# Performance work log

Measured on AMD Instinct MI355X. Metric: run time of the kernel, lower is better.

## Reference

```python
import jax, jax.numpy as jnp
import numpy as np

B, H, W, C = 8, 64, 64, 128
L = H * W
NH = 4
HD = C // NH
SCALE = HD ** -0.5
WIN = 8
SHIFT = 4
DEPTH = 2
K = 3
N = WIN * WIN
NW = (H // WIN) * (W // WIN)


def _rel_pos_index(win):
    coords = np.stack(np.meshgrid(np.arange(win), np.arange(win), indexing='ij'))
    cf = coords.reshape(2, -1)
    rel = (cf[:, :, None] - cf[:, None, :]).transpose(1, 2, 0).copy()
    rel[:, :, 0] += win - 1
    rel[:, :, 1] += win - 1
    rel[:, :, 0] *= 2 * win - 1
    return rel.sum(-1)  # (N, N)

REL_IDX = jnp.asarray(_rel_pos_index(WIN).reshape(-1))


def _attn_mask(Hh, Ww, win, shift):
    img = np.zeros((Hh, Ww))
    cnt = 0
    for hs in (slice(0, -win), slice(-win, -shift), slice(-shift, None)):
        for ws in (slice(0, -win), slice(-win, -shift), slice(-shift, None)):
            img[hs, ws] = cnt
            cnt += 1
    mw = img.reshape(Hh // win, win, Ww // win, win).transpose(0, 2, 1, 3).reshape(-1, win * win)
    m = mw[:, None, :] - mw[:, :, None]
    return jnp.asarray(np.where(m != 0, -100.0, 0.0).astype(np.float32))  # (nW, N, N)

ATTN_MASK = _attn_mask(H, W, WIN, SHIFT)


def layer_norm(x, g, b, eps=1e-5):
    mu = x.mean(-1, keepdims=True)
    var = x.var(-1, keepdims=True)
    return (x - mu) / jnp.sqrt(var + eps) * g + b


def window_partition(x, win):
    Bb, Hh, Ww, Cc = x.shape
    x = x.reshape(Bb, Hh // win, win, Ww // win, win, Cc)
    return x.transpose(0, 1, 3, 2, 4, 5).reshape(-1, win, win, Cc)


def window_reverse(wins, win, Hh, Ww):
    Bb = wins.shape[0] // (Hh * Ww // win // win)
    x = wins.reshape(Bb, Hh // win, Ww // win, win, win, -1)
    return x.transpose(0, 1, 3, 2, 4, 5).reshape(Bb, Hh, Ww, -1)


def swin_block(x, shift, n1g, n1b, qkvw, qkvb, rp, pw, pb, n2g, n2b, f1w, f1b, f2w, f2b):
    shortcut = x
    x = layer_norm(x, n1g, n1b).reshape(B, H, W, C)
    if shift > 0:
        x = jnp.roll(x, (-shift, -shift), axis=(1, 2))
    xw = window_partition(x, WIN).reshape(-1, N, C)  # (B*nW, N, C)
    qkv = (xw @ qkvw + qkvb).reshape(-1, N, 3, NH, HD).transpose(2, 0, 3, 1, 4)
    q, k, v = qkv[0] * SCALE, qkv[1], qkv[2]
    attn = jnp.einsum('whnd,whmd->whnm', q, k)  # (B*nW, NH, N, N)
    bias = rp[REL_IDX].reshape(N, N, NH).transpose(2, 0, 1)
    attn = attn + bias[None]
    if shift > 0:
        attn = (attn.reshape(B, NW, NH, N, N) + ATTN_MASK[None, :, None]).reshape(-1, NH, N, N)
    attn = jax.nn.softmax(attn, axis=-1)
    out = jnp.einsum('whnm,whmd->whnd', attn, v).transpose(0, 2, 1, 3).reshape(-1, N, C)
    out = out @ pw + pb
    x = window_reverse(out.reshape(-1, WIN, WIN, C), WIN, H, W)
    if shift > 0:
        x = jnp.roll(x, (shift, shift), axis=(1, 2))
    x = shortcut + x.reshape(B, L, C)
    h = layer_norm(x, n2g, n2b)
    h = jax.nn.gelu(h @ f1w + f1b, approximate=False) @ f2w + f2b
    return x + h


def conv1d(x, w, b):  # x (B,C,L), w (O,I,K)
    y = jax.lax.conv_general_dilated(x, w, (1,), [(K // 2, K // 2)], dimension_numbers=('NCH', 'OIH', 'NCH'))
    return y + b[None, :, None]


def deform_conv1d(xt, off_w, off_b, msk_w, msk_b):
    x = xt.transpose(0, 2, 1)  # (B, C, L)
    offset = conv1d(x, off_w, off_b)                    # (B, K, L)
    mask = jax.nn.sigmoid(conv1d(x, msk_w, msk_b))      # (B, K, L)
    i = jnp.arange(L, dtype=x.dtype)
    pos = jnp.clip(i[None, None, :] + offset, 0.0, L - 1)  # (B, K, L)
    fp = jnp.floor(pos).astype(jnp.int32)
    cp = jnp.minimum(fp + 1, L - 1)
    alpha = pos - fp.astype(x.dtype)
    idx_f = jnp.broadcast_to(fp[:, None], (B, C, K, L))
    idx_c = jnp.broadcast_to(cp[:, None], (B, C, K, L))
    xe = jnp.broadcast_to(x[:, :, None, :], (B, C, K, L))
    xf = jnp.take_along_axis(xe, idx_f, axis=3)
    xc = jnp.take_along_axis(xe, idx_c, axis=3)
    samp = xf * (1.0 - alpha[:, None]) + xc * alpha[:, None]
    out = (samp * mask[:, None]).sum(2)  # (B, C, L)
    # faithful to torch: output.view(B, L, out_channels) reinterprets memory, no transpose
    return out.reshape(B, L, C)


def _forward(xt, hx, cx, red_w, red_b, n1g, n1b, qkvw, qkvb, rp, pw, pb, n2g, n2b,
             f1w, f1b, f2w, f2b, off_w, off_b, msk_w, msk_b, lf_w, lf_b, gf_w, gf_b, ff_w, ff_b):
    # global branch: inject hidden state then W-MSA / SW-MSA blocks
    g = jnp.concatenate([xt, hx], axis=-1) @ red_w + red_b
    for i, shift in enumerate((0, SHIFT)):
        g = swin_block(g, shift, n1g[i], n1b[i], qkvw[i], qkvb[i], rp[i], pw[i], pb[i],
                       n2g[i], n2b[i], f1w[i], f1b[i], f2w[i], f2b[i])
    # local branch: deformable 1D conv over token axis
    local = deform_conv1d(xt, off_w, off_b, msk_w, msk_b)
    # local-global fusion
    fu = jax.nn.relu((local @ lf_w + lf_b) * (g @ gf_w + gf_b)) @ ff_w + ff_b
    # LSTM-style gating (SwinLSTM cell update)
    gate = jax.nn.sigmoid(fu)
    cell = jnp.tanh(fu)
    cy = gate * (cx + cell)
    hy = gate * jnp.tanh(cy)
    return hy


def setup_inputs():
    key = jax.random.key(0)
    ks = iter(jax.random.split(key, 24))
    def rn(shape, s=0.02):
        return jax.random.normal(next(ks), shape, jnp.float32) * s
    return dict(
        xt=jax.random.normal(next(ks), (B, L, C), jnp.float32),
        hx=jax.random.normal(next(ks), (B, L, C), jnp.float32),
        cx=jax.random.normal(next(ks), (B, L, C), jnp.float32),
        red_w=rn((2 * C, C)), red_b=jnp.zeros((C,), jnp.float32),
        n1g=jnp.ones((DEPTH, C), jnp.float32), n1b=jnp.zeros((DEPTH, C), jnp.float32),
        qkvw=rn((DEPTH, C, 3 * C)), qkvb=jnp.zeros((DEPTH, 3 * C), jnp.float32),
        rp=rn((DEPTH, (2 * WIN - 1) ** 2, NH)),
        pw=rn((DEPTH, C, C)), pb=jnp.zeros((DEPTH, C), jnp.float32),
        n2g=jnp.ones((DEPTH, C), jnp.float32), n2b=jnp.zeros((DEPTH, C), jnp.float32),
        f1w=rn((DEPTH, C, 4 * C)), f1b=jnp.zeros((DEPTH, 4 * C), jnp.float32),
        f2w=rn((DEPTH, 4 * C, C)), f2b=jnp.zeros((DEPTH, C), jnp.float32),
        off_w=rn((K, C, K)), off_b=jnp.zeros((K,), jnp.float32),
        msk_w=rn((K, C, K)), msk_b=jnp.zeros((K,), jnp.float32),
        lf_w=rn((C, C)), lf_b=jnp.zeros((C,), jnp.float32),
        gf_w=rn((C, C)), gf_b=jnp.zeros((C,), jnp.float32),
        ff_w=rn((C, C)), ff_b=jnp.zeros((C,), jnp.float32),
    )


def reference(xt, hx, cx, red_w, red_b, n1g, n1b, qkvw, qkvb, rp, pw, pb, n2g, n2b,
              f1w, f1b, f2w, f2b, off_w, off_b, msk_w, msk_b, lf_w, lf_b, gf_w, gf_b, ff_w, ff_b):
    return _forward(xt, hx, cx, red_w, red_b, n1g, n1b, qkvw, qkvb, rp, pw, pb, n2g, n2b,
                    f1w, f1b, f2w, f2b, off_w, off_b, msk_w, msk_b, lf_w, lf_b, gf_w, gf_b, ff_w, ff_b)
```

## Files before the change

kernel.cpp:

```cpp
#include <hip/hip_runtime.h>
#include <hip/hip_bf16.h>
#include <math.h>

typedef __hip_bfloat16 bf16;
typedef unsigned short u16;
#define BF(x) __bfloat162float(x)
static __device__ __forceinline__ bf16 FB(float x) { return __float2bfloat16(x); }
static __device__ __forceinline__ u16 FBu(float x) {
    bf16 b = __float2bfloat16(x);
    return *(u16*)&b;
}

typedef __attribute__((ext_vector_type(4))) float f32x4;
typedef __attribute__((ext_vector_type(8))) __bf16 bf16x8;


#define O_REDW 0
#define O_QKVW 32768
#define O_PW   131072
#define O_F1W  163840
#define O_F2W  294912
#define O_LFW  425984
#define O_GFW  442368
#define O_FFW  458752
#define O_REDB 475136
#define O_QKVB 475264
#define O_PB   476032
#define O_F1B  476288
#define O_F2B  477312
#define O_LFB  477568
#define O_GFB  477696
#define O_FFB  477824
#define O_RP   477952
#define O_N1G  479752
#define O_N1B  480008
#define O_N2G  480264
#define O_N2B  480520
#define O_OW   480776
#define O_OB   481928
#define O_MW   481931
#define O_MB   483083

#define ROW_S 36
#define CH_S  2320
#define CH32_S 1168

__device__ __forceinline__ int get_mode(const void* xt) {
    const unsigned* w = (const unsigned*)xt;
    int zlo = 0, inband = 0;
    #pragma unroll
    for (int i = 0; i < 32; ++i) {
        unsigned lo = w[i] & 0xFFFFu;
        int e = (int)((lo >> 7) & 0xFF);
        zlo += (lo == 0u || lo == 0x8000u);
        inband += (e >= 100 && e <= 140);
    }
    if (zlo >= 29) return 1;
    return (inband >= 20) ? 0 : 1;
}

__device__ __forceinline__ float LD(const void* p, size_t i, int mode) {
    return mode ? ((const float*)p)[i] : BF(((const bf16*)p)[i]);
}

__device__ __forceinline__ void async16(const u16* g, u16* l) {
    __builtin_amdgcn_global_load_lds(
        (const __attribute__((address_space(1))) unsigned int*)g,
        (__attribute__((address_space(3))) unsigned int*)l, 16, 0, 0);
}

struct PrepT { const void* src; int srcOff, K, N, dstOff; };
struct Prep { PrepT d[29]; int start[30]; };

__global__ void prep_k(Prep p, bf16* __restrict__ dst, const void* __restrict__ dtp) {
    const int mode = get_mode(dtp);
    int i = blockIdx.x * 256 + threadIdx.x;
    if (i >= p.start[29]) return;
    int s = 0;
    while (p.start[s + 1] <= i) ++s;
    int e = i - p.start[s];
    float v;
    if (p.d[s].N > 0) {
        int n = e / p.d[s].K, k = e % p.d[s].K;
        v = LD(p.d[s].src, (size_t)p.d[s].srcOff + (size_t)k * p.d[s].N + n, mode);
    } else {
        v = LD(p.d[s].src, (size_t)p.d[s].srcOff + e, mode);
    }
    dst[p.d[s].dstOff + e] = FB(v);
}

__launch_bounds__(256)
__global__ void xcat_k(const void* __restrict__ xt, const void* __restrict__ hx,
                       u16* __restrict__ X) {
    const int mode = get_mode(xt);
    const int total = 32768 * 32;
    for (int gidx = blockIdx.x * 256 + threadIdx.x; gidx < total;
         gidx += gridDim.x * 256) {
        int r = gidx >> 5, gi = gidx & 31;
        const void* src = (gi < 16) ? xt : hx;
        int c = (gi & 15) << 3;
        u16 outv[8];
        if (mode) {
            const float* s = (const float*)src + (size_t)r * 128 + c;
            float4 a = *(const float4*)s;
            float4 b = *(const float4*)(s + 4);
            outv[0] = FBu(a.x); outv[1] = FBu(a.y); outv[2] = FBu(a.z); outv[3] = FBu(a.w);
            outv[4] = FBu(b.x); outv[5] = FBu(b.y); outv[6] = FBu(b.z); outv[7] = FBu(b.w);
        } else {
            *(uint4*)outv = *(const uint4*)((const u16*)src + (size_t)r * 128 + c);
        }
        *(uint4*)(X + (size_t)r * 256 + (gi << 3)) = *(const uint4*)outv;
    }
}

template <int EPI>
__launch_bounds__(256)
__global__ void gemm_mfma(const u16* __restrict__ A, const u16* __restrict__ Bt,
                          const bf16* __restrict__ bias, bf16* __restrict__ outb,
                          float* __restrict__ outf, int M, int N, int K, int shift) {
    __shared__ __align__(16) u16 Als[2][2048];
    __shared__ __align__(16) u16 Bls[2][4096];
    const int tid = threadIdx.x;
    const int wave = tid >> 6, lane = tid & 63;
    const int q = lane >> 4, lr = lane & 15;
    const int wm = (wave >> 1) << 5, wn = (wave & 1) << 6;
    const int bm = blockIdx.y << 6, bn = blockIdx.x << 7;
    const f32x4 zero = {0.f, 0.f, 0.f, 0.f};
    f32x4 acc[2][4];
    #pragma unroll
    for (int i = 0; i < 2; ++i)
        #pragma unroll
        for (int j = 0; j < 4; ++j) acc[i][j] = zero;

    const int nk = K >> 5;
    {
        int c = tid;
        async16(A + (size_t)(bm + (c >> 2)) * K + ((c & 3) << 3), Als[0] + (c << 3));
        #pragma unroll
        for (int c2 = tid; c2 < 512; c2 += 256)
            async16(Bt + (size_t)(bn + (c2 >> 2)) * K + ((c2 & 3) << 3), Bls[0] + (c2 << 3));
    }
    __syncthreads();

    for (int i = 0; i < nk; ++i) {
        const int cur = i & 1, nxt = cur ^ 1;
        if (i + 1 < nk) {
            int k1 = (i + 1) << 5;
            int c = tid;
            async16(A + (size_t)(bm + (c >> 2)) * K + k1 + ((c & 3) << 3), Als[nxt] + (c << 3));
            #pragma unroll
            for (int c2 = tid; c2 < 512; c2 += 256)
                async16(Bt + (size_t)(bn + (c2 >> 2)) * K + k1 + ((c2 & 3) << 3), Bls[nxt] + (c2 << 3));
        }
        bf16x8 af[2], bfr[4];
        #pragma unroll
        for (int t = 0; t < 2; ++t)
            af[t] = *(const bf16x8*)(Als[cur] + ((wm + (t << 4) + lr) << 5) + (q << 3));
        #pragma unroll
        for (int t = 0; t < 4; ++t)
            bfr[t] = *(const bf16x8*)(Bls[cur] + ((wn + (t << 4) + lr) << 5) + (q << 3));
        #pragma unroll
        for (int mt = 0; mt < 2; ++mt)
            #pragma unroll
            for (int nt = 0; nt < 4; ++nt)
                acc[mt][nt] = __builtin_amdgcn_mfma_f32_16x16x32_bf16(
                    af[mt], bfr[nt], acc[mt][nt], 0, 0, 0);
        __syncthreads();
    }

    #pragma unroll
    for (int nt = 0; nt < 4; ++nt) {
        int col = bn + wn + (nt << 4) + lr;
        float bv = BF(bias[col]);
        #pragma unroll
        for (int mt = 0; mt < 2; ++mt) {
            int row0 = bm + wm + (mt << 4) + (q << 2);
            #pragma unroll
            for (int i = 0; i < 4; ++i) {
                int r = row0 + i;
                float v = acc[mt][nt][i] + bv;
                size_t idx = (size_t)r * N + col;
                if (EPI == 0) {
                    outb[idx] = FB(v);
                } else if (EPI == 3) {
                    int b = r >> 12, rem = r & 4095;
                    int wi = rem >> 6, n = rem & 63;
                    int hp = ((wi >> 3) << 3) + (n >> 3);
                    int wp = ((wi & 7) << 3) + (n & 7);
                    int h = (hp + shift) & 63, w = (wp + shift) & 63;
                    outf[((size_t)((b << 12) + (h << 6) + w)) * 128 + col] += v;
                } else if (EPI == 5) {
                    outf[idx] = v;
                }
            }
        }
    }
}

__launch_bounds__(256)
__global__ void qkvln_k(const float* __restrict__ g, const u16* __restrict__ wtu,
                        const bf16* __restrict__ wtb, u16* __restrict__ qkv,
                        int d, int shift) {
    __shared__ __align__(16) u16 Ach[4 * CH_S];
    __shared__ __align__(16) u16 Bb[2][8192];
    const int tid = threadIdx.x;
    const int wave = tid >> 6, lane = tid & 63;
    const int q = lane >> 4, lr = lane & 15;
    const int wm = (wave >> 1) << 5, wn = (wave & 1) << 6;
    const int bm = blockIdx.x << 6;
    const u16* Wq = wtu + O_QKVW + d * 49152;

    #pragma unroll
    for (int i = tid; i < 1024; i += 256) {
        int kc = i >> 9, c = i & 511;
        async16(Wq + (size_t)(c >> 2) * 128 + (kc << 5) + ((c & 3) << 3),
                Bb[0] + (kc << 12) + (c << 3));
    }

    {
        int row = tid >> 2, qtr = tid & 3;
        int r = bm + row;
        int b = r >> 12, rem = r & 4095;
        int wi = rem >> 6, n = rem & 63;
        int hp = ((wi >> 3) << 3) + (n >> 3);
        int wp = ((wi & 7) << 3) + (n & 7);
        int h = (hp + shift) & 63, w = (wp + shift) & 63;
        int src = (b << 12) + (h << 6) + w;
        const float* gr = g + (size_t)src * 128 + qtr * 32;
        float vals[32];
        float s1 = 0.f, s2 = 0.f;
        #pragma unroll
        for (int i = 0; i < 8; ++i) {
            float4 v4 = *(const float4*)(gr + i * 4);
            vals[i * 4] = v4.x; vals[i * 4 + 1] = v4.y;
            vals[i * 4 + 2] = v4.z; vals[i * 4 + 3] = v4.w;
            s1 += v4.x + v4.y + v4.z + v4.w;
            s2 += v4.x * v4.x + v4.y * v4.y + v4.z * v4.z + v4.w * v4.w;
        }
        s1 += __shfl_xor(s1, 1); s1 += __shfl_xor(s1, 2);
        s2 += __shfl_xor(s2, 1); s2 += __shfl_xor(s2, 2);
        float mu = s1 * (1.f / 128.f);
        float var = s2 * (1.f / 128.f) - mu * mu;
        float inv = rsqrtf(var + 1e-5f);
        #pragma unroll
        for (int i = 0; i < 32; ++i) {
            int c = qtr * 32 + i;
            float o = (vals[i] - mu) * inv * BF(wtb[O_N1G + d * 128 + c])
                      + BF(wtb[O_N1B + d * 128 + c]);
            Ach[qtr * CH_S + row * ROW_S + i] = FBu(o);
        }
    }
    __syncthreads();

    const f32x4 zero = {0.f, 0.f, 0.f, 0.f};
    f32x4 acc[2][4];
    for (int s = 0; s < 6; ++s) {
        const int nc = s >> 1, kh = s & 1;
        const int bsel = s & 1;
        if (s < 5) {
            int t = s + 1, nct = t >> 1, kht = t & 1;
            const u16* Bg = Wq + nct * 16384;
            #pragma unroll
            for (int i = tid; i < 1024; i += 256) {
                int kc = i >> 9, c = i & 511;
                async16(Bg + (size_t)(c >> 2) * 128 + (kht << 6) + (kc << 5) + ((c & 3) << 3),
                        Bb[t & 1] + (kc << 12) + (c << 3));
            }
        }
        if (kh == 0) {
            #pragma unroll
            for (int i = 0; i < 2; ++i)
                #pragma unroll
                for (int j = 0; j < 4; ++j) acc[i][j] = zero;
        }
        #pragma unroll
        for (int kc = 0; kc < 2; ++kc) {
            bf16x8 af[2], bfr[4];
            #pragma unroll
            for (int t = 0; t < 2; ++t)
                af[t] = *(const bf16x8*)(Ach + (2 * kh + kc) * CH_S + (wm + (t << 4) + lr) * ROW_S + (q << 3));
            #pragma unroll
            for (int t = 0; t < 4; ++t)
                bfr[t] = *(const bf16x8*)(Bb[bsel] + (kc << 12) + ((wn + (t << 4) + lr) << 5) + (q << 3));
            #pragma unroll
            for (int mt = 0; mt < 2; ++mt)
                #pragma unroll
                for (int nt = 0; nt < 4; ++nt)
                    acc[mt][nt] = __builtin_amdgcn_mfma_f32_16x16x32_bf16(
                        af[mt], bfr[nt], acc[mt][nt], 0, 0, 0);
        }
        if (kh == 1) {
            #pragma unroll
            for (int nt = 0; nt < 4; ++nt) {
                int col = wn + (nt << 4) + lr;
                float bv = BF(wtb[O_QKVB + d * 384 + nc * 128 + col]);
                #pragma unroll
                for (int mt = 0; mt < 2; ++mt) {
                    #pragma unroll
                    for (int i = 0; i < 4; ++i) {
                        int r = bm + wm + (mt << 4) + (q << 2) + i;
                        qkv[(size_t)r * 384 + nc * 128 + col] = FBu(acc[mt][nt][i] + bv);
                    }
                }
            }
        }
        if (s < 5) __syncthreads();
    }
}

__launch_bounds__(256, 2)
__global__ void attn_k(const u16* __restrict__ qkv, const bf16* __restrict__ rp,
                       u16* __restrict__ outp, int shift) {
    __shared__ __align__(16) u16 vT[4][32][72];
    __shared__ __align__(16) u16 pbuf[4][64][72];
    const int wq = blockIdx.x;
    const int head = threadIdx.x >> 6;
    const int lane = threadIdx.x & 63;
    const int q8 = lane >> 4, lr = lane & 15;
    const size_t base = (size_t)wq * 64;
    const f32x4 zero = {0.f, 0.f, 0.f, 0.f};

    #pragma unroll
    for (int j = 0; j < 4; ++j) {
        bf16x8 vv = *(const bf16x8*)(qkv + (base + lane) * 384 + 256 + head * 32 + j * 8);
        #pragma unroll
        for (int e = 0; e < 8; ++e) vT[head][j * 8 + e][lane] = ((const u16*)&vv)[e];
    }

    bf16x8 af[4], bfk[4];
    #pragma unroll
    for (int t = 0; t < 4; ++t) {
        af[t]  = *(const bf16x8*)(qkv + (base + t * 16 + lr) * 384 + head * 32 + q8 * 8);
        bfk[t] = *(const bf16x8*)(qkv + (base + t * 16 + lr) * 384 + 128 + head * 32 + q8 * 8);
    }
    f32x4 accs[4][4];
    #pragma unroll
    for (int rt = 0; rt < 4; ++rt)
        #pragma unroll
        for (int ct = 0; ct < 4; ++ct) accs[rt][ct] = zero;
    #pragma unroll
    for (int rt = 0; rt < 4; ++rt)
        #pragma unroll
        for (int ct = 0; ct < 4; ++ct)
            accs[rt][ct] = __builtin_amdgcn_mfma_f32_16x16x32_bf16(
                af[rt], bfk[ct], accs[rt][ct], 0, 0, 0);

    const int wloc = wq & 63;
    const int wh = (wloc >> 3) << 3, wwb = (wloc & 7) << 3;
    #pragma unroll
    for (int rt = 0; rt < 4; ++rt) {
        #pragma unroll
        for (int i = 0; i < 4; ++i) {
            int r = rt * 16 + q8 * 4 + i;
            int ti = r >> 3, tj = r & 7;
            int regt = 0;
            if (shift) {
                int hp = wh + ti, wp = wwb + tj;
                int rh = hp < 56 ? 0 : (hp < 60 ? 1 : 2);
                int rw = wp < 56 ? 0 : (wp < 60 ? 1 : 2);
                regt = rh * 3 + rw;
            }
            float sv[4];
            float mx = -1e30f;
            #pragma unroll
            for (int ct = 0; ct < 4; ++ct) {
                int m = ct * 16 + lr;
                float a = accs[rt][ct][i] * 0.17677669529663687f;
                int idx = (ti - (m >> 3) + 7) * 15 + (tj - (m & 7) + 7);
                a += BF(rp[idx * 4 + head]);
                if (shift) {
                    int hp = wh + (m >> 3), wp = wwb + (m & 7);
                    int rh = hp < 56 ? 0 : (hp < 60 ? 1 : 2);
                    int rw = wp < 56 ? 0 : (wp < 60 ? 1 : 2);
                    if (regt != rh * 3 + rw) a -= 100.f;
                }
                sv[ct] = a;
                mx = fmaxf(mx, a);
            }
            mx = fmaxf(mx, __shfl_xor(mx, 1));
            mx = fmaxf(mx, __shfl_xor(mx, 2));
            mx = fmaxf(mx, __shfl_xor(mx, 4));
            mx = fmaxf(mx, __shfl_xor(mx, 8));
            float l = 0.f;
            #pragma unroll
            for (int ct = 0; ct < 4; ++ct) { sv[ct] = expf(sv[ct] - mx); l += sv[ct]; }
            l += __shfl_xor(l, 1); l += __shfl_xor(l, 2);
            l += __shfl_xor(l, 4); l += __shfl_xor(l, 8);
            float inv = 1.f / l;
            #pragma unroll
            for (int ct = 0; ct < 4; ++ct)
                pbuf[head][r][ct * 16 + lr] = FBu(sv[ct] * inv);
        }
    }

    f32x4 acco[4][2];
    #pragma unroll
    for (int rt = 0; rt < 4; ++rt) { acco[rt][0] = zero; acco[rt][1] = zero; }
    #pragma unroll
    for (int mh = 0; mh < 2; ++mh) {
        bf16x8 vb[2];
        #pragma unroll
        for (int dt = 0; dt < 2; ++dt)
            vb[dt] = *(const bf16x8*)(&vT[head][dt * 16 + lr][mh * 32 + q8 * 8]);
        #pragma unroll
        for (int rt = 0; rt < 4; ++rt) {
            bf16x8 pa = *(const bf16x8*)(&pbuf[head][rt * 16 + lr][mh * 32 + q8 * 8]);
            #pragma unroll
            for (int dt = 0; dt < 2; ++dt)
                acco[rt][dt] = __builtin_amdgcn_mfma_f32_16x16x32_bf16(
                    pa, vb[dt], acco[rt][dt], 0, 0, 0);
        }
    }

    #pragma unroll
    for (int rt = 0; rt < 4; ++rt)
        #pragma unroll
        for (int dt = 0; dt < 2; ++dt)
            #pragma unroll
            for (int i = 0; i < 4; ++i) {
                int r = rt * 16 + q8 * 4 + i;
                outp[(base + r) * 128 + head * 32 + dt * 16 + lr] = FBu(acco[rt][dt][i]);
            }
}

__launch_bounds__(256)
__global__ void mlp_k(float* __restrict__ g, bf16* __restrict__ gbf,
                      const u16* __restrict__ wtu, const bf16* __restrict__ wtb,
                      int d) {
    __shared__ __align__(16) u16 Ach[4 * CH_S];
    __shared__ __align__(16) u16 bufB1[8192];
    __shared__ __align__(16) u16 bufB2[8192];
    __shared__ __align__(16) u16 buf2[2 * CH_S];
    const int tid = threadIdx.x;
    const int wave = tid >> 6, lane = tid & 63;
    const int q = lane >> 4, lr = lane & 15;
    const int wm = (wave >> 1) << 5;
    const int wn0 = (wave & 1) << 5;
    const int wn = (wave & 1) << 6;
    const int bm = blockIdx.x << 6;

    {
        const u16* B1g = wtu + O_F1W + d * 65536;
        #pragma unroll
        for (int i = tid; i < 1024; i += 256) {
            int kc = i >> 8, c = i & 255;
            async16(B1g + (c >> 2) * 128 + (kc << 5) + ((c & 3) << 3),
                    bufB1 + (kc << 11) + (c << 3));
        }
    }

    {
        int row = tid >> 2, qtr = tid & 3;
        const float* gr = g + (size_t)(bm + row) * 128 + qtr * 32;
        float vals[32];
        float s1 = 0.f, s2 = 0.f;
        #pragma unroll
        for (int i = 0; i < 8; ++i) {
            float4 v4 = *(const float4*)(gr + i * 4);
            vals[i * 4] = v4.x; vals[i * 4 + 1] = v4.y;
            vals[i * 4 + 2] = v4.z; vals[i * 4 + 3] = v4.w;
            s1 += v4.x + v4.y + v4.z + v4.w;
            s2 += v4.x * v4.x + v4.y * v4.y + v4.z * v4.z + v4.w * v4.w;
        }
        s1 += __shfl_xor(s1, 1); s1 += __shfl_xor(s1, 2);
        s2 += __shfl_xor(s2, 1); s2 += __shfl_xor(s2, 2);
        float mu = s1 * (1.f / 128.f);
        float var = s2 * (1.f / 128.f) - mu * mu;
        float inv = rsqrtf(var + 1e-5f);
        #pragma unroll
        for (int i = 0; i < 32; ++i) {
            int c = qtr * 32 + i;
            float o = (vals[i] - mu) * inv * BF(wtb[O_N2G + d * 128 + c])
                      + BF(wtb[O_N2B + d * 128 + c]);
            Ach[qtr * CH_S + row * ROW_S + i] = FBu(o);
        }
    }
    __syncthreads();

    const f32x4 zero = {0.f, 0.f, 0.f, 0.f};
    f32x4 acc2[2][4];
    #pragma unroll
    for (int i = 0; i < 2; ++i)
        #pragma unroll
        for (int j = 0; j < 4; ++j) acc2[i][j] = zero;

    for (int h = 0; h < 8; ++h) {
        {
            const u16* B2g = wtu + O_F2W + d * 65536 + h * 64;
            #pragma unroll
            for (int i = tid; i < 1024; i += 256) {
                int kc = i >> 9, c = i & 511;
                async16(B2g + (size_t)(c >> 2) * 512 + (kc << 5) + ((c & 3) << 3),
                        bufB2 + (kc << 12) + (c << 3));
            }
        }
        f32x4 acc1[2][2];
        #pragma unroll
        for (int i = 0; i < 2; ++i) { acc1[i][0] = zero; acc1[i][1] = zero; }
        #pragma unroll
        for (int k0 = 0; k0 < 4; ++k0) {
            bf16x8 af[2], bfr[2];
            #pragma unroll
            for (int t = 0; t < 2; ++t) {
                af[t]  = *(const bf16x8*)(Ach + k0 * CH_S + (wm + (t << 4) + lr) * ROW_S + (q << 3));
                bfr[t] = *(const bf16x8*)(bufB1 + (k0 << 11) + ((wn0 + (t << 4) + lr) << 5) + (q << 3));
            }
            #pragma unroll
            for (int mt = 0; mt < 2; ++mt)
                #pragma unroll
                for (int nt = 0; nt < 2; ++nt)
                    acc1[mt][nt] = __builtin_amdgcn_mfma_f32_16x16x32_bf16(
                        af[mt], bfr[nt], acc1[mt][nt], 0, 0, 0);
        }
        #pragma unroll
        for (int nt = 0; nt < 2; ++nt) {
            int c = wn0 + (nt << 4) + lr;
            float hb = BF(wtb[O_F1B + d * 512 + h * 64 + c]);
            #pragma unroll
            for (int mt = 0; mt < 2; ++mt) {
                #pragma unroll
                for (int i = 0; i < 4; ++i) {
                    int r = wm + (mt << 4) + (q << 2) + i;
                    float v = acc1[mt][nt][i] + hb;
                    float ge = 0.5f * v * (1.0f + erff(v * 0.70710678118654752f));
                    buf2[(c >> 5) * CH_S + r * ROW_S + (c & 31)] = FBu(ge);
                }
            }
        }
        __syncthreads();
        if (h < 7) {
            const u16* B1g = wtu + O_F1W + d * 65536 + (h + 1) * 8192;
            #pragma unroll
            for (int i = tid; i < 1024; i += 256) {
                int kc = i >> 8, c = i & 255;
                async16(B1g + (c >> 2) * 128 + (kc << 5) + ((c & 3) << 3),
                        bufB1 + (kc << 11) + (c << 3));
            }
        }
        #pragma unroll
        for (int kc = 0; kc < 2; ++kc) {
            bf16x8 ah[2], b2[4];
            #pragma unroll
            for (int t = 0; t < 2; ++t)
                ah[t] = *(const bf16x8*)(buf2 + kc * CH_S + (wm + (t << 4) + lr) * ROW_S + (q << 3));
            #pragma unroll
            for (int t = 0; t < 4; ++t)
                b2[t] = *(const bf16x8*)(bufB2 + (kc << 12) + ((wn + (t << 4) + lr) << 5) + (q << 3));
            #pragma unroll
            for (int mt = 0; mt < 2; ++mt)
                #pragma unroll
                for (int nt = 0; nt < 4; ++nt)
                    acc2[mt][nt] = __builtin_amdgcn_mfma_f32_16x16x32_bf16(
                        ah[mt], b2[nt], acc2[mt][nt], 0, 0, 0);
        }
        __syncthreads();
    }
    #pragma unroll
    for (int nt = 0; nt < 4; ++nt) {
        int col = wn + (nt << 4) + lr;
        float bv = BF(wtb[O_F2B + d * 128 + col]);
        #pragma unroll
        for (int mt = 0; mt < 2; ++mt) {
            #pragma unroll
            for (int i = 0; i < 4; ++i) {
                int r = bm + wm + (mt << 4) + (q << 2) + i;
                size_t idx = (size_t)r * 128 + col;
                float nv = g[idx] + acc2[mt][nt][i] + bv;
                g[idx] = nv;
                gbf[idx] = FB(nv);
            }
        }
    }
}

__launch_bounds__(256, 4)
__global__ void fuse3_k(const u16* __restrict__ Aloc, const u16* __restrict__ Ag,
                        const u16* __restrict__ wtu, const bf16* __restrict__ wtb,
                        const void* __restrict__ cx, void* __restrict__ out,
                        const void* __restrict__ dtp) {
    __shared__ __align__(16) u16 relb[4 * CH32_S];
    const int mode = get_mode(dtp);
    const int tid = threadIdx.x;
    const int wave = tid >> 6, lane = tid & 63;
    const int q = lane >> 4, lr = lane & 15;
    const int wn = wave << 5;
    const int bm = blockIdx.x << 5;
    const f32x4 zero = {0.f, 0.f, 0.f, 0.f};
    f32x4 acc1[2][2], acc2[2][2];
    #pragma unroll
    for (int i = 0; i < 2; ++i)
        #pragma unroll
        for (int j = 0; j < 2; ++j) { acc1[i][j] = zero; acc2[i][j] = zero; }

    #pragma unroll
    for (int k0 = 0; k0 < 4; ++k0) {
        bf16x8 al[2], ag[2], blf[2], bgf[2];
        #pragma unroll
        for (int t = 0; t < 2; ++t) {
            size_t off = (size_t)(bm + (t << 4) + lr) * 128 + (k0 << 5) + (q << 3);
            al[t] = *(const bf16x8*)(Aloc + off);
            ag[t] = *(const bf16x8*)(Ag + off);
        }
        #pragma unroll
        for (int t = 0; t < 2; ++t) {
            int woff = ((wn + (t << 4) + lr) << 7) + (k0 << 5) + (q << 3);
            blf[t] = *(const bf16x8*)(wtu + O_LFW + woff);
            bgf[t] = *(const bf16x8*)(wtu + O_GFW + woff);
        }
        #pragma unroll
        for (int mt = 0; mt < 2; ++mt)
            #pragma unroll
            for (int nt = 0; nt < 2; ++nt) {
                acc1[mt][nt] = __builtin_amdgcn_mfma_f32_16x16x32_bf16(
                    al[mt], blf[nt], acc1[mt][nt], 0, 0, 0);
                acc2[mt][nt] = __builtin_amdgcn_mfma_f32_16x16x32_bf16(
                    ag[mt], bgf[nt], acc2[mt][nt], 0, 0, 0);
            }
    }
    #pragma unroll
    for (int nt = 0; nt < 2; ++nt) {
        int c = wn + (nt << 4) + lr;
        float lfb = BF(wtb[O_LFB + c]);
        float gfb = BF(wtb[O_GFB + c]);
        #pragma unroll
        for (int mt = 0; mt < 2; ++mt) {
            #pragma unroll
            for (int i = 0; i < 4; ++i) {
                int r = (mt << 4) + (q << 2) + i;
                float t1 = acc1[mt][nt][i] + lfb;
                float t2 = acc2[mt][nt][i] + gfb;
                float rel = t1 * t2;
                relb[(c >> 5) * CH32_S + r * ROW_S + (c & 31)] = FBu(rel > 0.f ? rel : 0.f);
            }
        }
    }
    __syncthreads();
    f32x4 acc3[2][2];
    #pragma unroll
    for (int i = 0; i < 2; ++i)
        #pragma unroll
        for (int j = 0; j < 2; ++j) acc3[i][j] = zero;
    #pragma unroll
    for (int k0 = 0; k0 < 4; ++k0) {
        bf16x8 ar[2], bff[2];
        #pragma unroll
        for (int t = 0; t < 2; ++t)
            ar[t] = *(const bf16x8*)(relb + k0 * CH32_S + ((t << 4) + lr) * ROW_S + (q << 3));
        #pragma unroll
        for (int t = 0; t < 2; ++t)
            bff[t] = *(const bf16x8*)(wtu + O_FFW + ((wn + (t << 4) + lr) << 7) + (k0 << 5) + (q << 3));
        #pragma unroll
        for (int mt = 0; mt < 2; ++mt)
            #pragma unroll
            for (int nt = 0; nt < 2; ++nt)
                acc3[mt][nt] = __builtin_amdgcn_mfma_f32_16x16x32_bf16(
                    ar[mt], bff[nt], acc3[mt][nt], 0, 0, 0);
    }
    #pragma unroll
    for (int nt = 0; nt < 2; ++nt) {
        int col = wn + (nt << 4) + lr;
        float ffb = BF(wtb[O_FFB + col]);
        #pragma unroll
        for (int mt = 0; mt < 2; ++mt) {
            #pragma unroll
            for (int i = 0; i < 4; ++i) {
                int r = bm + (mt << 4) + (q << 2) + i;
                size_t idx = (size_t)r * 128 + col;
                float v = acc3[mt][nt][i] + ffb;
                float gate = 1.f / (1.f + expf(-v));
                float cell = tanhf(v);
                float cy = gate * (LD(cx, idx, mode) + cell);
                float hy = gate * tanhf(cy);
                if (mode) ((float*)out)[idx] = hy;
                else      ((bf16*)out)[idx] = FB(hy);
            }
        }
    }
}

__launch_bounds__(256)
__global__ void offmask_k(const void* __restrict__ xt, const bf16* __restrict__ wtb,
                          float4* __restrict__ om) {
    const int mode = get_mode(xt);
    const int wave = threadIdx.x >> 6, lane = threadIdx.x & 63;
    const int gl = blockIdx.x * 4 + wave;
    const int b = gl >> 12, l = gl & 4095;
    float wo[3][3][2], wmk[3][3][2];
    #pragma unroll
    for (int k = 0; k < 3; ++k)
        #pragma unroll
        for (int j = 0; j < 3; ++j) {
            wo[k][j][0]  = BF(wtb[O_OW + (k * 128 + lane) * 3 + j]);
            wo[k][j][1]  = BF(wtb[O_OW + (k * 128 + lane + 64) * 3 + j]);
            wmk[k][j][0] = BF(wtb[O_MW + (k * 128 + lane) * 3 + j]);
            wmk[k][j][1] = BF(wtb[O_MW + (k * 128 + lane + 64) * 3 + j]);
        }
    float a6[6] = {};
    #pragma unroll
    for (int j = 0; j < 3; ++j) {
        int row = l + j - 1;
        if (row >= 0 && row < 4096) {
            size_t base = ((size_t)(b << 12) + row) * 128;
            float x0 = LD(xt, base + lane, mode);
            float x1 = LD(xt, base + lane + 64, mode);
            #pragma unroll
            for (int k = 0; k < 3; ++k) {
                a6[k]     += x0 * wo[k][j][0]  + x1 * wo[k][j][1];
                a6[3 + k] += x0 * wmk[k][j][0] + x1 * wmk[k][j][1];
            }
        }
    }
    #pragma unroll
    for (int off = 32; off > 0; off >>= 1)
        #pragma unroll
        for (int k = 0; k < 6; ++k) a6[k] += __shfl_down(a6[k], off);
    if (lane == 0) {
        #pragma unroll
        for (int k = 0; k < 3; ++k) {
            float off = a6[k] + BF(wtb[O_OB + k]);
            float pos = fminf(fmaxf((float)l + off, 0.f), 4095.f);
            float fpf = floorf(pos);
            float mv = a6[3 + k] + BF(wtb[O_MB + k]);
            float mk = 1.f / (1.f + expf(-mv));
            om[(size_t)gl * 3 + k] = make_float4(fpf, pos - fpf, mk, 0.f);
        }
    }
}

__launch_bounds__(512)
__global__ void sample_k(const void* __restrict__ xt, const float4* __restrict__ om,
                         bf16* __restrict__ outL) {
    __shared__ __align__(16) u16 ot[128 * 72];
    const int mode = get_mode(xt);
    const int tid = threadIdx.x;
    const int b = blockIdx.x >> 6;
    const int l0 = (blockIdx.x & 63) << 6;
    const int c = tid & 127, lh = tid >> 7;
    for (int it = 0; it < 16; ++it) {
        int l_loc = lh * 16 + it;
        size_t gl = (size_t)(b << 12) + l0 + l_loc;
        float o = 0.f;
        #pragma unroll
        for (int k = 0; k < 3; ++k) {
            float4 v = om[gl * 3 + k];
            int fp = (int)v.x;
            int cp = fp + 1 > 4095 ? 4095 : fp + 1;
            float al = v.y, mk = v.z;
            float xf = LD(xt, ((size_t)(b << 12) + fp) * 128 + c, mode);
            float xc = LD(xt, ((size_t)(b << 12) + cp) * 128 + c, mode);
            o += (xf * (1.f - al) + xc * al) * mk;
        }
        ot[c * 72 + l_loc] = FBu(o);
    }
    __syncthreads();
    #pragma unroll
    for (int pass = 0; pass < 2; ++pass) {
        int cc = pass * 64 + (tid >> 3);
        int oo = tid & 7;
        const uint4 v = *(const uint4*)(ot + cc * 72 + oo * 8);
        *(uint4*)(outL + (size_t)b * 524288 + (size_t)cc * 4096 + l0 + oo * 8) = v;
    }
}

extern "C" void kernel_launch(void* const* d_in, const int* in_sizes, int n_in,
                              void* d_out, int out_size, void* d_ws, size_t ws_size,
                              hipStream_t stream) {
    (void)out_size; (void)ws_size;
    int I[28] = {0,1,2,3,4,5,6,7,8,9,10,11,12,13,14,15,16,17,18,19,20,21,22,23,24,25,26,27};
    if (n_in >= 28 && in_sizes[7] != 98304 && in_sizes[23] == 98304 && in_sizes[26] == 1800) {
        int alt[28] = {27, 9, 0, 25, 24, 15, 14, 23, 22, 26, 21, 20, 17, 16,
                       2, 1, 4, 3, 19, 18, 13, 12, 11, 10, 8, 7, 6, 5};
        for (int i = 0; i < 28; ++i) I[i] = alt[i];
    }
    const void* xt = d_in[I[0]];
    const void* hx = d_in[I[1]];
    const void* cx = d_in[I[2]];

    char* wsb = (char*)d_ws;
    float* g    = (float*)wsb;
    u16*   Abf  = (u16*)(wsb + 16777216);
    u16*   Bbf  = (u16*)(wsb + 25165824);
    u16*   Cbf  = (u16*)(wsb + 50331648);
    bf16*  wtb  = (bf16*)(wsb + 58720256);
    u16*   wtu  = (u16*)wtb;
    float4* om  = (float4*)(wsb + 25165824);

    Prep p;
    PrepT descs[29] = {
        {d_in[I[3]],  0,     256, 128, O_REDW},
        {d_in[I[7]],  0,     128, 384, O_QKVW},
        {d_in[I[7]],  49152, 128, 384, O_QKVW + 49152},
        {d_in[I[10]], 0,     128, 128, O_PW},
        {d_in[I[10]], 16384, 128, 128, O_PW + 16384},
        {d_in[I[14]], 0,     128, 512, O_F1W},
        {d_in[I[14]], 65536, 128, 512, O_F1W + 65536},
        {d_in[I[16]], 0,     512, 128, O_F2W},
        {d_in[I[16]], 65536, 512, 128, O_F2W + 65536},
        {d_in[I[22]], 0,     128, 128, O_LFW},
        {d_in[I[24]], 0,     128, 128, O_GFW},
        {d_in[I[26]], 0,     128, 128, O_FFW},
        {d_in[I[4]],  0,  128, 0, O_REDB},
        {d_in[I[8]],  0,  768, 0, O_QKVB},
        {d_in[I[11]], 0,  256, 0, O_PB},
        {d_in[I[15]], 0, 1024, 0, O_F1B},
        {d_in[I[17]], 0,  256, 0, O_F2B},
        {d_in[I[23]], 0,  128, 0, O_LFB},
        {d_in[I[25]], 0,  128, 0, O_GFB},
        {d_in[I[27]], 0,  128, 0, O_FFB},
        {d_in[I[9]],  0, 1800, 0, O_RP},
        {d_in[I[5]],  0,  256, 0, O_N1G},
        {d_in[I[6]],  0,  256, 0, O_N1B},
        {d_in[I[12]], 0,  256, 0, O_N2G},
        {d_in[I[13]], 0,  256, 0, O_N2B},
        {d_in[I[18]], 0, 1152, 0, O_OW},
        {d_in[I[19]], 0,    3, 0, O_OB},
        {d_in[I[20]], 0, 1152, 0, O_MW},
        {d_in[I[21]], 0,    3, 0, O_MB},
    };
    int cum = 0;
    for (int i = 0; i < 29; ++i) {
        p.d[i] = descs[i];
        p.start[i] = cum;
        cum += (descs[i].N > 0) ? descs[i].K * descs[i].N : descs[i].K;
    }
    p.start[29] = cum;

    prep_k<<<(cum + 255) / 256, 256, 0, stream>>>(p, wtb, xt);
    xcat_k<<<1024, 256, 0, stream>>>(xt, hx, Bbf);

    gemm_mfma<5><<<dim3(1, 512), 256, 0, stream>>>(Bbf, wtu + O_REDW, wtb + O_REDB,
                                                   nullptr, g, 32768, 128, 256, 0);

    for (int d = 0; d < 2; ++d) {
        int shift = d ? 4 : 0;
        qkvln_k<<<512, 256, 0, stream>>>(g, wtu, wtb, Bbf, d, shift);
        attn_k<<<512, 256, 0, stream>>>(Bbf, wtb + O_RP + d * 900, Cbf, shift);
        gemm_mfma<3><<<dim3(1, 512), 256, 0, stream>>>(Cbf, wtu + O_PW + d * 16384,
                                                       wtb + O_PB + d * 128, nullptr, g,
                                                       32768, 128, 128, shift);
        mlp_k<<<512, 256, 0, stream>>>(g, (bf16*)Abf, wtu, wtb, d);
    }

    offmask_k<<<8192, 256, 0, stream>>>(xt, wtb, om);
    sample_k<<<512, 512, 0, stream>>>(xt, om, (bf16*)Cbf);
    fuse3_k<<<1024, 256, 0, stream>>>(Cbf, Abf, wtu, wtb, cx, d_out, xt);
}
```

Baseline: 404.9 us.

## Fuse attention output projection and residual scatter into attention kernel

The attention kernel now writes its per-head output into shared memory, syncs, and runs the output projection GEMM (128x128 weights) in-block, then adds bias and scatters the result with the window-reverse/unshift mapping directly into the fp32 residual. This removes the separate projection GEMM launch and the global round trip of the attention output. The cost is extra work and shared-memory use per attention block, plus projection weights read from global memory by every block. ROW_S must be defined elsewhere, and pbuf now uses a flat 4608-element per-head layout.

```diff
diff --git a/kernel.cpp b/kernel.cpp
--- a/kernel.cpp
+++ b/kernel.cpp
@@ -182,13 +182,6 @@
                 size_t idx = (size_t)r * N + col;
                 if (EPI == 0) {
                     outb[idx] = FB(v);
-                } else if (EPI == 3) {
-                    int b = r >> 12, rem = r & 4095;
-                    int wi = rem >> 6, n = rem & 63;
-                    int hp = ((wi >> 3) << 3) + (n >> 3);
-                    int wp = ((wi & 7) << 3) + (n & 7);
-                    int h = (hp + shift) & 63, w = (wp + shift) & 63;
-                    outf[((size_t)((b << 12) + (h << 6) + w)) * 128 + col] += v;
                 } else if (EPI == 5) {
                     outf[idx] = v;
                 }
@@ -309,10 +302,12 @@
 }
 
 __launch_bounds__(256, 2)
-__global__ void attn_k(const u16* __restrict__ qkv, const bf16* __restrict__ rp,
-                       u16* __restrict__ outp, int shift) {
+__global__ void attn_k(const u16* __restrict__ qkv, const u16* __restrict__ wtu,
+                       const bf16* __restrict__ wtb, float* __restrict__ g,
+                       int d, int shift) {
     __shared__ __align__(16) u16 vT[4][32][72];
-    __shared__ __align__(16) u16 pbuf[4][64][72];
+    __shared__ __align__(16) u16 pbuf[4][4608];
+    const bf16* rp = wtb + O_RP + d * 900;
     const int wq = blockIdx.x;
     const int head = threadIdx.x >> 6;
     const int lane = threadIdx.x & 63;
@@ -389,7 +384,7 @@
             float inv = 1.f / l;
             #pragma unroll
             for (int ct = 0; ct < 4; ++ct)
-                pbuf[head][r][ct * 16 + lr] = FBu(sv[ct] * inv);
+                pbuf[head][r * 72 + ct * 16 + lr] = FBu(sv[ct] * inv);
         }
     }
 
@@ -404,7 +399,7 @@
             vb[dt] = *(const bf16x8*)(&vT[head][dt * 16 + lr][mh * 32 + q8 * 8]);
         #pragma unroll
         for (int rt = 0; rt < 4; ++rt) {
-            bf16x8 pa = *(const bf16x8*)(&pbuf[head][rt * 16 + lr][mh * 32 + q8 * 8]);
+            bf16x8 pa = *(const bf16x8*)(&pbuf[head][(rt * 16 + lr) * 72 + mh * 32 + q8 * 8]);
             #pragma unroll
             for (int dt = 0; dt < 2; ++dt)
                 acco[rt][dt] = __builtin_amdgcn_mfma_f32_16x16x32_bf16(
@@ -419,8 +414,50 @@
             #pragma unroll
             for (int i = 0; i < 4; ++i) {
                 int r = rt * 16 + q8 * 4 + i;
-                outp[(base + r) * 128 + head * 32 + dt * 16 + lr] = FBu(acco[rt][dt][i]);
-            }
+                pbuf[head][r * ROW_S + dt * 16 + lr] = FBu(acco[rt][dt][i]);
+            }
+    __syncthreads();
+
+    const u16* Wp = wtu + O_PW + d * 16384;
+    const int wn = head << 5;
+    f32x4 accp[4][2];
+    #pragma unroll
+    for (int rt = 0; rt < 4; ++rt) { accp[rt][0] = zero; accp[rt][1] = zero; }
+    #pragma unroll
+    for (int k0 = 0; k0 < 4; ++k0) {
+        bf16x8 ap[4], bp[2];
+        #pragma unroll
+        for (int rt = 0; rt < 4; ++rt)
+            ap[rt] = *(const bf16x8*)(&pbuf[k0][(rt * 16 + lr) * ROW_S + q8 * 8]);
+        #pragma unroll
+        for (int nt = 0; nt < 2; ++nt)
+            bp[nt] = *(const bf16x8*)(Wp + (size_t)(wn + (nt << 4) + lr) * 128 + (k0 << 5) + (q8 << 3));
+        #pragma unroll
+        for (int rt = 0; rt < 4; ++rt)
+            #pragma unroll
+            for (int nt = 0; nt < 2; ++nt)
+                accp[rt][nt] = __builtin_amdgcn_mfma_f32_16x16x32_bf16(
+                    ap[rt], bp[nt], accp[rt][nt], 0, 0, 0);
+    }
+    #pragma unroll
+    for (int nt = 0; nt < 2; ++nt) {
+        int col = wn + (nt << 4) + lr;
+        float bv = BF(wtb[O_PB + d * 128 + col]);
+        #pragma unroll
+        for (int rt = 0; rt < 4; ++rt) {
+            #pragma unroll
+            for (int i = 0; i < 4; ++i) {
+                int r = (int)base + rt * 16 + q8 * 4 + i;
+                float v = accp[rt][nt][i] + bv;
+                int b = r >> 12, rem = r & 4095;
+                int wi = rem >> 6, n = rem & 63;
+                int hp = ((wi >> 3) << 3) + (n >> 3);
+                int wp = ((wi & 7) << 3) + (n & 7);
+                int h = (hp + shift) & 63, w = (wp + shift) & 63;
+                g[((size_t)((b << 12) + (h << 6) + w)) * 128 + col] += v;
+            }
+        }
+    }
 }
 
 __launch_bounds__(256)
@@ -834,10 +871,7 @@
     for (int d = 0; d < 2; ++d) {
         int shift = d ? 4 : 0;
         qkvln_k<<<512, 256, 0, stream>>>(g, wtu, wtb, Bbf, d, shift);
-        attn_k<<<512, 256, 0, stream>>>(Bbf, wtb + O_RP + d * 900, Cbf, shift);
-        gemm_mfma<3><<<dim3(1, 512), 256, 0, stream>>>(Cbf, wtu + O_PW + d * 16384,
-                                                       wtb + O_PB + d * 128, nullptr, g,
-                                                       32768, 128, 128, shift);
+        attn_k<<<512, 256, 0, stream>>>(Bbf, wtu, wtb, g, d, shift);
         mlp_k<<<512, 256, 0, stream>>>(g, (bf16*)Abf, wtu, wtb, d);
     }
 
```

Measured after the change: 401.7 us. No clear change (-0.8%).
